# Performance work log

Hardware: AMD Instinct MI355X
Metric: run time of the kernel (lower is better)

The kernel has to match this reference:

```python
import jax, jax.numpy as jnp
import numpy as np

N = 200000      # nodes per graph
E = 6400000     # edges per graph
F_IN = 100      # node feature dim (GCNConv(100,16))
HID = 16
NC = 2
STRIDE = 20     # log_softmax(...)[::20]
M = N // STRIDE # rows fed to the MLP head


def _gcn(x, src, dst, W1, b1, W2, b2):
    """PyG-style GCNConv x2: add self loops, sym-normalize, linear -> aggregate -> bias."""
    n = x.shape[0]
    loops = jnp.arange(n)
    s = jnp.concatenate([src, loops])
    d = jnp.concatenate([dst, loops])
    deg = jax.ops.segment_sum(jnp.ones(s.shape[0], dtype=x.dtype), d, num_segments=n)
    dinv = jnp.where(deg > 0, jax.lax.rsqrt(deg), 0.0)
    norm = (dinv[s] * dinv[d])[:, None]  # [E+n, 1]
    h = x @ W1                                    # [n, 16]
    h = jax.ops.segment_sum(norm * h[s], d, num_segments=n) + b1
    h = jax.nn.relu(h)  # dropout is identity in eval mode
    h = h @ W2                                    # [n, 2]
    h = jax.ops.segment_sum(norm * h[s], d, num_segments=n) + b2
    return jax.nn.log_softmax(h, axis=1)[::STRIDE]  # [n/20, 2]


def setup_inputs() -> dict:
    key = jax.random.key(0)
    ks = jax.random.split(key, 24)
    inp = {
        'batch1_edge_index': jax.random.randint(ks[0], (2, E), 0, N),
        'batch1_x': jax.random.normal(ks[1], (N, F_IN), dtype=jnp.float32),
        'batch2_edge_index': jax.random.randint(ks[2], (2, E), 0, N),
        'batch2_x': jax.random.normal(ks[3], (N, F_IN), dtype=jnp.float32),
        'transE_input': jax.random.uniform(ks[4], (M,), dtype=jnp.float32),
        'ComplEx_input': jax.random.uniform(ks[5], (M,), dtype=jnp.float32),
        'path_input': jax.random.uniform(ks[6], (M,), dtype=jnp.float32),
        'edit_input': jax.random.uniform(ks[7], (M,), dtype=jnp.float32),
    }
    s = 0.1
    inp['gh_W1'] = jax.random.normal(ks[8], (F_IN, HID), dtype=jnp.float32) * s
    inp['gh_b1'] = jnp.zeros((HID,), dtype=jnp.float32)
    inp['gh_W2'] = jax.random.normal(ks[9], (HID, NC), dtype=jnp.float32) * s
    inp['gh_b2'] = jnp.zeros((NC,), dtype=jnp.float32)
    inp['gt_W1'] = jax.random.normal(ks[10], (F_IN, HID), dtype=jnp.float32) * s
    inp['gt_b1'] = jnp.zeros((HID,), dtype=jnp.float32)
    inp['gt_W2'] = jax.random.normal(ks[11], (HID, NC), dtype=jnp.float32) * s
    inp['gt_b2'] = jnp.zeros((NC,), dtype=jnp.float32)
    inp['m_W1'] = jax.random.normal(ks[12], (5, 80), dtype=jnp.float32) * s
    inp['m_b1'] = jnp.zeros((80,), dtype=jnp.float32)
    inp['m_W2'] = jax.random.normal(ks[13], (80, 10), dtype=jnp.float32) * s
    inp['m_b2'] = jnp.zeros((10,), dtype=jnp.float32)
    inp['m_W3'] = jax.random.normal(ks[14], (10, 1), dtype=jnp.float32) * s
    inp['m_b3'] = jnp.zeros((1,), dtype=jnp.float32)
    return inp


def reference(batch1_edge_index, batch1_x, batch2_edge_index, batch2_x,
              transE_input, ComplEx_input, path_input, edit_input,
              gh_W1, gh_b1, gh_W2, gh_b2,
              gt_W1, gt_b1, gt_W2, gt_b2,
              m_W1, m_b1, m_W2, m_b2, m_W3, m_b3):
    gcnh_out = _gcn(batch1_x, batch1_edge_index[0], batch1_edge_index[1],
                    gh_W1, gh_b1, gh_W2, gh_b2)
    # gcnt_out is computed in the original forward but never used in the output
    gcnt_out = _gcn(batch2_x, batch2_edge_index[0], batch2_edge_index[1],
                    gt_W1, gt_b1, gt_W2, gt_b2)
    BP_input = jnp.concatenate(
        [transE_input[:, None], ComplEx_input[:, None], path_input[:, None], gcnh_out], axis=1)  # [M, 5]
    # NOTE: original computes mean/std normalization then OVERWRITES it with
    # min_max_normalize(BP_input); we faithfully apply only global min-max.
    mn, mx = jnp.min(BP_input), jnp.max(BP_input)
    BP_norm = (BP_input - mn) / (mx - mn)
    h = jax.nn.relu(BP_norm @ m_W1 + m_b1)
    h = jax.nn.relu(h @ m_W2 + m_b2)
    out = jax.nn.sigmoid(h @ m_W3 + m_b3)  # [M, 1]
    return out
```

## Files before the change

kernel.cpp:

```cpp
#include <hip/hip_runtime.h>
#include <math.h>

#define NN 200000
#define NE 6400000
#define FIN 100
#define MR 10000
#define BSH 14
#define NBK 13
#define NSB 1563
#define EPB 4096
#define CAP1E 544768
#define SBB 133
#define CAP2E 4864
#define SCAP 360448
#define STCAP 5120

static __device__ __forceinline__ unsigned enc_f(float f){
  unsigned u = __float_as_uint(f);
  return (u & 0x80000000u) ? ~u : (u | 0x80000000u);
}
static __device__ __forceinline__ float dec_f(unsigned u){
  return (u & 0x80000000u) ? __uint_as_float(u ^ 0x80000000u) : __uint_as_float(~u);
}
static __device__ __forceinline__ unsigned short f2bf(float f){
  unsigned u = __float_as_uint(f);
  return (unsigned short)((u + 0x7fffu + ((u >> 16) & 1u)) >> 16);
}
static __device__ __forceinline__ float bf2f(unsigned short h){
  return __uint_as_float(((unsigned)h) << 16);
}

__global__ void k_init(int* bcur1, int* bcur2, float* gacc, unsigned* mm, unsigned* scnt){
  int i = blockIdx.x*blockDim.x + threadIdx.x;
  if(i < NBK) bcur1[i] = i*CAP1E;
  if(i < NSB) bcur2[i] = i*CAP2E;
  if(i < 2*MR) gacc[i] = 0.f;
  if(i == 0){ mm[0] = 0xFFFFFFFFu; mm[1] = 0u; scnt[0] = 0u; }
}

__global__ __launch_bounds__(256) void k_stageA(const int* __restrict__ src,
                                                const int* __restrict__ dst,
                                                int* __restrict__ bcur1,
                                                unsigned* __restrict__ bucket1){
  __shared__ unsigned stage[EPB];
  __shared__ unsigned char binOf[EPB];
  __shared__ int cnt[4][NBK];
  __shared__ int tot[NBK], bst[NBK], woff[4][NBK], gbase[NBK];
  int t = threadIdx.x;
  int w = t >> 6;
  int ebase = blockIdx.x*EPB;
  int nEdge = min(EPB, NE - ebase);
  if(t < 4*NBK) ((int*)cnt)[t] = 0;
  __syncthreads();
  unsigned pk[16]; int bb[16], rr[16];
  const int4* s4 = (const int4*)(src + ebase);
  const int4* d4 = (const int4*)(dst + ebase);
  #pragma unroll
  for(int j=0;j<4;j++){
    int q = t + j*256, eo = q*4;
    if(eo < nEdge){
      int4 s = s4[q]; int4 d = d4[q];
      int ds[4] = {d.x,d.y,d.z,d.w}, ss[4] = {s.x,s.y,s.z,s.w};
      #pragma unroll
      for(int k=0;k<4;k++){
        int b = ds[k]>>BSH;
        pk[j*4+k] = ((unsigned)(ds[k] & 16383) << 18) | (unsigned)ss[k];
        bb[j*4+k] = b;
        rr[j*4+k] = atomicAdd(&cnt[w][b], 1);
      }
    } else {
      rr[j*4+0]=rr[j*4+1]=rr[j*4+2]=rr[j*4+3] = -1;
    }
  }
  __syncthreads();
  if(t < NBK){
    int s = 0;
    #pragma unroll
    for(int wv=0; wv<4; wv++){ woff[wv][t] = s; s += cnt[wv][t]; }
    tot[t] = s;
  }
  __syncthreads();
  if(t == 0){
    int run = 0;
    #pragma unroll
    for(int b=0;b<NBK;b++){ bst[b] = run; run += tot[b]; }
  }
  __syncthreads();
  if(t < NBK && tot[t]) gbase[t] = atomicAdd(&bcur1[t], tot[t]);
  #pragma unroll
  for(int j=0;j<16;j++){
    if(rr[j] >= 0){
      int b = bb[j];
      int p = bst[b] + woff[w][b] + rr[j];
      stage[p] = pk[j]; binOf[p] = (unsigned char)b;
    }
  }
  __syncthreads();
  for(int k=t; k<nEdge; k+=256){
    int b = binOf[k];
    bucket1[gbase[b] + (k - bst[b])] = stage[k];
  }
}

__global__ __launch_bounds__(256) void k_stageB(const unsigned* __restrict__ bucket1,
                                                const int* __restrict__ bcur1,
                                                int* __restrict__ bcur2,
                                                unsigned* __restrict__ bucket2,
                                                unsigned* __restrict__ sed,
                                                unsigned* __restrict__ scnt){
  __shared__ unsigned stage[EPB];
  __shared__ unsigned char binOf[EPB];
  __shared__ int cnt[128], bst[128], gbase[128];
  __shared__ unsigned sbuf[384];
  __shared__ int slds, sgbase;
  int t = threadIdx.x;
  int b = blockIdx.x / SBB;
  int chunk = blockIdx.x % SBB;
  int cntb = bcur1[b] - b*CAP1E;
  int el = chunk*EPB;
  int nEdge = min(EPB, cntb - el);
  if(nEdge <= 0) return;
  if(t < 128) cnt[t] = 0;
  if(t == 0) slds = 0;
  __syncthreads();
  int t20 = (20 - (4*b) % 20) % 20;
  unsigned pk2[16]; int ln[16], rr[16];
  const uint4* e4 = (const uint4*)(bucket1 + (size_t)b*CAP1E + el);
  #pragma unroll
  for(int j=0;j<4;j++){
    int q = t + j*256, eo = q*4;
    uint4 e = make_uint4(0,0,0,0);
    if(eo < nEdge) e = e4[q];
    unsigned ev[4] = {e.x, e.y, e.z, e.w};
    #pragma unroll
    for(int k=0;k<4;k++){
      int idx = j*4+k;
      if(eo + k < nEdge){
        unsigned p = ev[k];
        unsigned dl14 = p >> 18;
        int bin = (int)(dl14 >> 7);
        pk2[idx] = ((dl14 & 127u) << 18) | (p & 0x3FFFFu);
        ln[idx] = bin;
        rr[idx] = atomicAdd(&cnt[bin], 1);
        if((int)(dl14 % 20u) == t20){
          int sp = atomicAdd(&slds, 1);
          if(sp < 384){
            unsigned sidx = (unsigned)((b*16384 + (int)dl14) / 20);
            sbuf[sp] = (sidx << 18) | (p & 0x3FFFFu);
          }
        }
      } else rr[idx] = -1;
    }
  }
  __syncthreads();
  if(t == 0){
    int run = 0;
    for(int i=0;i<128;i++){ bst[i] = run; run += cnt[i]; }
    if(slds > 384) slds = 384;
    sgbase = (slds > 0) ? (int)atomicAdd(scnt, (unsigned)slds) : 0;
  }
  __syncthreads();
  if(t < 128 && cnt[t]){
    int sbg = (b<<7) + t;
    gbase[t] = atomicAdd(&bcur2[sbg], cnt[t]);
  }
  #pragma unroll
  for(int j=0;j<16;j++){
    if(rr[j] >= 0){
      int p = bst[ln[j]] + rr[j];
      stage[p] = pk2[j]; binOf[p] = (unsigned char)ln[j];
    }
  }
  __syncthreads();
  for(int k=t; k<nEdge; k+=256){
    int bin = binOf[k];
    bucket2[gbase[bin] + (k - bst[bin])] = stage[k];
  }
  for(int k=t; k<slds; k+=256){
    int gp = sgbase + k;
    if(gp < SCAP) sed[gp] = sbuf[k];
  }
}

__global__ __launch_bounds__(256) void k_cnt(const unsigned* __restrict__ bucket2,
                                             const int* __restrict__ bcur2,
                                             float* __restrict__ dinv){
  __shared__ int c[128];
  int sb = blockIdx.x, t = threadIdx.x;
  if(t < 128) c[t] = 0;
  __syncthreads();
  int e0 = sb*CAP2E, e1 = bcur2[sb];
  for(int i=e0+t; i<e1; i+=256){
    unsigned pkv = bucket2[i];
    atomicAdd(&c[pkv>>18], 1);
  }
  __syncthreads();
  if(t < 128){
    int g = sb*128 + t;
    if(g < NN) dinv[g] = rsqrtf((float)(c[t] + 1));
  }
}

__global__ __launch_bounds__(256) void k_xw1(const float* __restrict__ x,
                                             const float* __restrict__ W1,
                                             const float* __restrict__ dinv,
                                             unsigned short* __restrict__ h1b){
  int row = blockIdx.x*256 + threadIdx.x;
  if(row >= NN) return;
  const float4* xr = (const float4*)(x + (size_t)row*FIN);
  float acc[16];
  #pragma unroll
  for(int c=0;c<16;c++) acc[c] = 0.f;
  #pragma unroll 5
  for(int kk=0;kk<25;kk++){
    float4 xv = xr[kk];
    const float* w = W1 + kk*4*16;
    #pragma unroll
    for(int c=0;c<16;c++){
      acc[c] += xv.x*w[c] + xv.y*w[16+c] + xv.z*w[32+c] + xv.w*w[48+c];
    }
  }
  float dv = dinv[row];
  unsigned p[8];
  #pragma unroll
  for(int c=0;c<8;c++){
    p[c] = (unsigned)f2bf(acc[2*c]*dv) | ((unsigned)f2bf(acc[2*c+1]*dv) << 16);
  }
  uint4* o = (uint4*)(h1b + (size_t)row*16);
  o[0] = make_uint4(p[0],p[1],p[2],p[3]);
  o[1] = make_uint4(p[4],p[5],p[6],p[7]);
}

__global__ __launch_bounds__(512) void k_aggfused(const unsigned* __restrict__ bucket2,
                                                  const int* __restrict__ bcur2,
                                                  const float* __restrict__ dinv,
                                                  const unsigned short* __restrict__ h1b,
                                                  const float* __restrict__ b1,
                                                  const float* __restrict__ W2,
                                                  float* __restrict__ h2s){
  __shared__ unsigned srt[STCAP];
  __shared__ int cnt[128], coff[129], cur[128];
  __shared__ int wsum0;
  int t = threadIdx.x, sb = blockIdx.x;
  int e0 = sb*CAP2E, e1 = bcur2[sb];
  int n  = e1 - e0;
  bool ok = (n <= STCAP);
  if(t < 128) cnt[t] = 0;
  __syncthreads();

  if(ok){
    unsigned er[10];
    #pragma unroll
    for(int k=0;k<10;k++){
      int i = e0 + t + k*512;
      if(i < e1){
        unsigned p = bucket2[i];
        er[k] = p;
        atomicAdd(&cnt[p>>18], 1);
      } else er[k] = 0xFFFFFFFFu;
    }
    __syncthreads();
    int v = (t<128) ? cnt[t] : 0;
    int s = v;
    #pragma unroll
    for(int o=1;o<64;o<<=1){
      int u = __shfl_up(s, o, 64);
      if((t&63) >= o) s += u;
    }
    if(t == 63) wsum0 = s;
    __syncthreads();
    if(t < 128){
      int ex = s - v + ((t>=64) ? wsum0 : 0);
      coff[t] = ex; cur[t] = ex;
    }
    if(t == 0) coff[128] = n;
    __syncthreads();
    #pragma unroll
    for(int k=0;k<10;k++){
      if(er[k] != 0xFFFFFFFFu){
        int p = atomicAdd(&cur[er[k]>>18], 1);
        srt[p] = er[k] & 0x3FFFFu;
      }
    }
    __syncthreads();
    int grp = t>>3, f2 = t&7;
    const unsigned* h1u = (const unsigned*)h1b;
    for(int nd=grp; nd<128; nd+=64){
      int g = sb*128 + nd;
      if(g >= NN) continue;
      int s0 = coff[nd], s1 = coff[nd+1];
      unsigned su = h1u[(size_t)g*8 + f2];
      float acc0 = bf2f((unsigned short)su);
      float acc1 = bf2f((unsigned short)(su>>16));
      int j = s0;
      for(; j+4 <= s1; j+=4){
        unsigned a0=srt[j], a1=srt[j+1], a2=srt[j+2], a3=srt[j+3];
        unsigned u0 = h1u[a0*8+f2], u1 = h1u[a1*8+f2];
        unsigned u2 = h1u[a2*8+f2], u3 = h1u[a3*8+f2];
        acc0 += (bf2f((unsigned short)u0) + bf2f((unsigned short)u1))
              + (bf2f((unsigned short)u2) + bf2f((unsigned short)u3));
        acc1 += (bf2f((unsigned short)(u0>>16)) + bf2f((unsigned short)(u1>>16)))
              + (bf2f((unsigned short)(u2>>16)) + bf2f((unsigned short)(u3>>16)));
      }
      for(; j<s1; j++){
        unsigned u = h1u[srt[j]*8+f2];
        acc0 += bf2f((unsigned short)u);
        acc1 += bf2f((unsigned short)(u>>16));
      }
      float dvd = dinv[g];
      float r0 = fmaxf(dvd*acc0 + b1[2*f2],   0.f);
      float r1 = fmaxf(dvd*acc1 + b1[2*f2+1], 0.f);
      float p0 = r0*W2[(2*f2)*2+0] + r1*W2[(2*f2+1)*2+0];
      float p1 = r0*W2[(2*f2)*2+1] + r1*W2[(2*f2+1)*2+1];
      #pragma unroll
      for(int o=4;o>0;o>>=1){
        p0 += __shfl_xor(p0, o, 8);
        p1 += __shfl_xor(p1, o, 8);
      }
      if(f2 == 0){
        h2s[g*2+0] = dvd * p0;
        h2s[g*2+1] = dvd * p1;
      }
    }
  } else {
    float* accf = (float*)srt;
    for(int i=t; i<2048; i+=512) accf[i] = 0.f;
    __syncthreads();
    int grp = t>>4, f = t&15;
    for(int i=e0+grp; i<e1; i+=32){
      unsigned pkv = bucket2[i];
      atomicAdd(&accf[(pkv>>18)*16 + f], bf2f(h1b[(size_t)(pkv & 0x3FFFFu)*16 + f]));
    }
    __syncthreads();
    for(int nd=grp; nd<128; nd+=32){
      int g = sb*128 + nd;
      if(g >= NN) continue;
      float dvd = dinv[g];
      float acc = accf[nd*16 + f] + bf2f(h1b[(size_t)g*16 + f]);
      float r = fmaxf(dvd*acc + b1[f], 0.f);
      float p0 = r * W2[f*2+0];
      float p1 = r * W2[f*2+1];
      #pragma unroll
      for(int o=8;o>0;o>>=1){
        p0 += __shfl_xor(p0, o, 16);
        p1 += __shfl_xor(p1, o, 16);
      }
      if(f == 0){
        h2s[g*2+0] = dvd * p0;
        h2s[g*2+1] = dvd * p1;
      }
    }
  }
}

__global__ __launch_bounds__(256) void k_agg2s(const unsigned* __restrict__ sed,
                                               const unsigned* __restrict__ scnt,
                                               const float* __restrict__ h2s,
                                               float* __restrict__ gacc){
  int total = (int)scnt[0];
  if(total > SCAP) total = SCAP;
  const float2* h2v = (const float2*)h2s;
  for(int i = blockIdx.x*256 + threadIdx.x; i < total; i += gridDim.x*256){
    unsigned p = sed[i];
    int idx = (int)(p >> 18);
    int srcn = (int)(p & 0x3FFFFu);
    float2 v = h2v[srcn];
    atomicAdd(&gacc[idx*2+0], v.x);
    atomicAdd(&gacc[idx*2+1], v.y);
  }
}

__global__ __launch_bounds__(256) void k_post(const float* __restrict__ gacc,
                                              const float* __restrict__ h2s,
                                              const float* __restrict__ dinv,
                                              const float* __restrict__ b2,
                                              const float* __restrict__ t1,
                                              const float* __restrict__ t2,
                                              const float* __restrict__ t3,
                                              float* __restrict__ gout,
                                              unsigned* __restrict__ mm){
  int i = blockIdx.x*256 + threadIdx.x;
  float lo = 3.4e38f, hi = -3.4e38f;
  if(i < MR){
    int g = i*20;
    float dvd = dinv[g];
    float o0 = dvd*(gacc[i*2+0] + h2s[g*2+0]) + b2[0];
    float o1 = dvd*(gacc[i*2+1] + h2s[g*2+1]) + b2[1];
    float m = fmaxf(o0, o1);
    float lse = m + logf(expf(o0-m) + expf(o1-m));
    float g0 = o0 - lse, g1 = o1 - lse;
    gout[i*2+0] = g0; gout[i*2+1] = g1;
    float a = t1[i], bb = t2[i], c = t3[i];
    lo = fminf(fminf(a,bb), fminf(c, fminf(g0,g1)));
    hi = fmaxf(fmaxf(a,bb), fmaxf(c, fmaxf(g0,g1)));
  }
  #pragma unroll
  for(int o=32;o>0;o>>=1){
    lo = fminf(lo, __shfl_xor(lo, o, 64));
    hi = fmaxf(hi, __shfl_xor(hi, o, 64));
  }
  __shared__ float slo[4], shi[4];
  int w = threadIdx.x >> 6, l = threadIdx.x & 63;
  if(l == 0){ slo[w] = lo; shi[w] = hi; }
  __syncthreads();
  if(threadIdx.x == 0){
    for(int j=1;j<4;j++){ lo = fminf(lo, slo[j]); hi = fmaxf(hi, shi[j]); }
    atomicMin(&mm[0], enc_f(lo));
    atomicMax(&mm[1], enc_f(hi));
  }
}

__global__ __launch_bounds__(256) void k_mlp(const float* __restrict__ t1, const float* __restrict__ t2,
                                             const float* __restrict__ t3, const float* __restrict__ g,
                                             const unsigned* __restrict__ mm,
                                             const float* __restrict__ W1, const float* __restrict__ b1,
                                             const float* __restrict__ W2, const float* __restrict__ b2,
                                             const float* __restrict__ W3, const float* __restrict__ b3,
                                             float* __restrict__ out){
  int i = blockIdx.x*256 + threadIdx.x;
  if(i >= MR) return;
  float mn = dec_f(mm[0]), mx = dec_f(mm[1]);
  float sc = 1.f/(mx - mn);
  float in[5];
  in[0] = (t1[i]   - mn)*sc;
  in[1] = (t2[i]   - mn)*sc;
  in[2] = (t3[i]   - mn)*sc;
  in[3] = (g[2*i]  - mn)*sc;
  in[4] = (g[2*i+1]- mn)*sc;
  float a[80];
  #pragma unroll
  for(int j=0;j<80;j++){
    float s = b1[j];
    #pragma unroll
    for(int k=0;k<5;k++) s += in[k]*W1[k*80+j];
    a[j] = fmaxf(s, 0.f);
  }
  float h[10];
  #pragma unroll
  for(int j=0;j<10;j++){
    float s = b2[j];
    #pragma unroll
    for(int k=0;k<80;k++) s += a[k]*W2[k*10+j];
    h[j] = fmaxf(s, 0.f);
  }
  float o = b3[0];
  #pragma unroll
  for(int k=0;k<10;k++) o += h[k]*W3[k];
  out[i] = 1.f/(1.f + expf(-o));
}

extern "C" void kernel_launch(void* const* d_in, const int* in_sizes, int n_in,
                              void* d_out, int out_size, void* d_ws, size_t ws_size,
                              hipStream_t stream) {
  (void)in_sizes; (void)n_in; (void)out_size; (void)ws_size;
  const int*   eidx    = (const int*)  d_in[0];
  const int*   src     = eidx;
  const int*   dst     = eidx + NE;
  const float* x       = (const float*)d_in[1];
  const float* transE  = (const float*)d_in[4];
  const float* ComplEx = (const float*)d_in[5];
  const float* path    = (const float*)d_in[6];
  const float* ghW1    = (const float*)d_in[8];
  const float* ghb1    = (const float*)d_in[9];
  const float* ghW2    = (const float*)d_in[10];
  const float* ghb2    = (const float*)d_in[11];
  const float* mW1     = (const float*)d_in[16];
  const float* mb1     = (const float*)d_in[17];
  const float* mW2     = (const float*)d_in[18];
  const float* mb2     = (const float*)d_in[19];
  const float* mW3     = (const float*)d_in[20];
  const float* mb3     = (const float*)d_in[21];
  float* out = (float*)d_out;

  char* w = (char*)d_ws;
  size_t off = 0;
  auto alloc = [&](size_t bytes)->void*{
    void* p = w + off;
    off += (bytes + 255) & ~(size_t)255;
    return p;
  };
  unsigned* bucket1 = (unsigned*)alloc((size_t)NBK*CAP1E*4);
  unsigned* bucket2 = (unsigned*)alloc((size_t)NSB*CAP2E*4);
  float*    dinv    = (float*)   alloc((size_t)NN*4);
  unsigned short* h1b = (unsigned short*)alloc((size_t)NN*16*2);
  float*    h2s     = (float*)   alloc((size_t)NN*2*4);
  float*    gacc    = (float*)   alloc((size_t)MR*2*4);
  float*    gout    = (float*)   alloc((size_t)MR*2*4);
  unsigned* sed     = (unsigned*)alloc((size_t)SCAP*4);
  int*      bcur1   = (int*)     alloc(64*4);
  int*      bcur2   = (int*)     alloc((size_t)(NSB+1)*4);
  unsigned* mm      = (unsigned*)alloc(256);
  unsigned* scnt    = (unsigned*)alloc(256);

  const int SA_BLOCKS = (NE + EPB - 1)/EPB;
  const int SB_BLOCKS = NBK*SBB;

  k_init    <<<(2*MR+255)/256, 256, 0, stream>>>(bcur1, bcur2, gacc, mm, scnt);
  k_stageA  <<<SA_BLOCKS, 256, 0, stream>>>(src, dst, bcur1, bucket1);
  k_stageB  <<<SB_BLOCKS, 256, 0, stream>>>(bucket1, bcur1, bcur2, bucket2, sed, scnt);
  k_cnt     <<<NSB, 256, 0, stream>>>(bucket2, bcur2, dinv);
  k_xw1     <<<(NN+255)/256, 256, 0, stream>>>(x, ghW1, dinv, h1b);
  k_aggfused<<<NSB, 512, 0, stream>>>(bucket2, bcur2, dinv, h1b, ghb1, ghW2, h2s);
  k_agg2s   <<<512, 256, 0, stream>>>(sed, scnt, h2s, gacc);
  k_post    <<<(MR+255)/256, 256, 0, stream>>>(gacc, h2s, dinv, ghb2,
                                               transE, ComplEx, path, gout, mm);
  k_mlp     <<<(MR+255)/256, 256, 0, stream>>>(transE, ComplEx, path, gout, mm,
                                               mW1, mb1, mW2, mb2, mW3, mb3, out);
}
```

Baseline: 445.6 us.

## Split bf16 node features into two 8-feature planes and gather them in two passes

The h1 feature table is stored as two separate planes of 8 bf16 features each (16 bytes per node per plane) instead of one interleaved 32-byte row. The fused aggregation gathers each plane in its own pass, with 4 lanes per node and an 8-way unrolled loop, so each pass touches a smaller working set that fits in cache better. k_xw1 now assigns 4 lanes per row, splitting the K dimension and combining partial sums with shuffles, which improves coalescing of x reads. The cost is a second gather pass over the edge list and an extra block barrier.

```diff
diff --git a/kernel.cpp b/kernel.cpp
--- a/kernel.cpp
+++ b/kernel.cpp
@@ -29,6 +29,8 @@
 static __device__ __forceinline__ float bf2f(unsigned short h){
   return __uint_as_float(((unsigned)h) << 16);
 }
+static __device__ __forceinline__ float bflo(unsigned u){ return bf2f((unsigned short)u); }
+static __device__ __forceinline__ float bfhi(unsigned u){ return bf2f((unsigned short)(u>>16)); }
 
 __global__ void k_init(int* bcur1, int* bcur2, float* gacc, unsigned* mm, unsigned* scnt){
   int i = blockIdx.x*blockDim.x + threadIdx.x;
@@ -205,30 +207,33 @@
                                              const float* __restrict__ W1,
                                              const float* __restrict__ dinv,
                                              unsigned short* __restrict__ h1b){
-  int row = blockIdx.x*256 + threadIdx.x;
+  int t = threadIdx.x;
+  int l = t & 3;
+  int row = blockIdx.x*64 + (t>>2);
   if(row >= NN) return;
   const float4* xr = (const float4*)(x + (size_t)row*FIN);
   float acc[16];
   #pragma unroll
   for(int c=0;c<16;c++) acc[c] = 0.f;
-  #pragma unroll 5
-  for(int kk=0;kk<25;kk++){
+  for(int kk=l; kk<25; kk+=4){
     float4 xv = xr[kk];
-    const float* w = W1 + kk*4*16;
+    const float* w = W1 + kk*64;
     #pragma unroll
     for(int c=0;c<16;c++){
       acc[c] += xv.x*w[c] + xv.y*w[16+c] + xv.z*w[32+c] + xv.w*w[48+c];
     }
   }
+  #pragma unroll
+  for(int o=2;o>0;o>>=1){
+    #pragma unroll
+    for(int c=0;c<16;c++) acc[c] += __shfl_xor(acc[c], o, 4);
+  }
   float dv = dinv[row];
-  unsigned p[8];
-  #pragma unroll
-  for(int c=0;c<8;c++){
-    p[c] = (unsigned)f2bf(acc[2*c]*dv) | ((unsigned)f2bf(acc[2*c+1]*dv) << 16);
-  }
-  uint4* o = (uint4*)(h1b + (size_t)row*16);
-  o[0] = make_uint4(p[0],p[1],p[2],p[3]);
-  o[1] = make_uint4(p[4],p[5],p[6],p[7]);
+  unsigned p0 = (unsigned)f2bf(acc[4*l]*dv)   | ((unsigned)f2bf(acc[4*l+1]*dv) << 16);
+  unsigned p1 = (unsigned)f2bf(acc[4*l+2]*dv) | ((unsigned)f2bf(acc[4*l+3]*dv) << 16);
+  unsigned* plane = (unsigned*)h1b + (size_t)(l>>1)*NN*4;
+  uint2* o2 = (uint2*)(plane + (size_t)row*4 + (l&1)*2);
+  *o2 = make_uint2(p0, p1);
 }
 
 __global__ __launch_bounds__(512) void k_aggfused(const unsigned* __restrict__ bucket2,
@@ -283,41 +288,81 @@
       }
     }
     __syncthreads();
-    int grp = t>>3, f2 = t&7;
-    const unsigned* h1u = (const unsigned*)h1b;
-    for(int nd=grp; nd<128; nd+=64){
-      int g = sb*128 + nd;
-      if(g >= NN) continue;
-      int s0 = coff[nd], s1 = coff[nd+1];
-      unsigned su = h1u[(size_t)g*8 + f2];
-      float acc0 = bf2f((unsigned short)su);
-      float acc1 = bf2f((unsigned short)(su>>16));
+
+    int grp = t>>2, f = t&3;
+    int g = sb*128 + grp;
+    bool live = (g < NN);
+    int s0 = 0, s1 = 0;
+    if(live){ s0 = coff[grp]; s1 = coff[grp+1]; }
+    float a00=0.f, a01=0.f, a10=0.f, a11=0.f;
+    const unsigned* h1u0 = (const unsigned*)h1b;
+    const unsigned* h1u1 = h1u0 + (size_t)NN*4;
+
+    if(live){
+      unsigned su = h1u0[(size_t)g*4 + f];
+      a00 = bflo(su); a01 = bfhi(su);
       int j = s0;
+      for(; j+8 <= s1; j+=8){
+        unsigned b0=srt[j],b1_=srt[j+1],b2=srt[j+2],b3=srt[j+3];
+        unsigned b4=srt[j+4],b5=srt[j+5],b6=srt[j+6],b7=srt[j+7];
+        unsigned u0=h1u0[b0*4+f], u1=h1u0[b1_*4+f], u2=h1u0[b2*4+f], u3=h1u0[b3*4+f];
+        unsigned u4=h1u0[b4*4+f], u5=h1u0[b5*4+f], u6=h1u0[b6*4+f], u7=h1u0[b7*4+f];
+        a00 += ((bflo(u0)+bflo(u1)) + (bflo(u2)+bflo(u3)))
+             + ((bflo(u4)+bflo(u5)) + (bflo(u6)+bflo(u7)));
+        a01 += ((bfhi(u0)+bfhi(u1)) + (bfhi(u2)+bfhi(u3)))
+             + ((bfhi(u4)+bfhi(u5)) + (bfhi(u6)+bfhi(u7)));
+      }
       for(; j+4 <= s1; j+=4){
-        unsigned a0=srt[j], a1=srt[j+1], a2=srt[j+2], a3=srt[j+3];
-        unsigned u0 = h1u[a0*8+f2], u1 = h1u[a1*8+f2];
-        unsigned u2 = h1u[a2*8+f2], u3 = h1u[a3*8+f2];
-        acc0 += (bf2f((unsigned short)u0) + bf2f((unsigned short)u1))
-              + (bf2f((unsigned short)u2) + bf2f((unsigned short)u3));
-        acc1 += (bf2f((unsigned short)(u0>>16)) + bf2f((unsigned short)(u1>>16)))
-              + (bf2f((unsigned short)(u2>>16)) + bf2f((unsigned short)(u3>>16)));
+        unsigned b0=srt[j],b1_=srt[j+1],b2=srt[j+2],b3=srt[j+3];
+        unsigned u0=h1u0[b0*4+f], u1=h1u0[b1_*4+f], u2=h1u0[b2*4+f], u3=h1u0[b3*4+f];
+        a00 += (bflo(u0)+bflo(u1)) + (bflo(u2)+bflo(u3));
+        a01 += (bfhi(u0)+bfhi(u1)) + (bfhi(u2)+bfhi(u3));
       }
       for(; j<s1; j++){
-        unsigned u = h1u[srt[j]*8+f2];
-        acc0 += bf2f((unsigned short)u);
-        acc1 += bf2f((unsigned short)(u>>16));
+        unsigned u = h1u0[srt[j]*4+f];
+        a00 += bflo(u); a01 += bfhi(u);
+      }
+    }
+    __syncthreads();
+    if(live){
+      unsigned su = h1u1[(size_t)g*4 + f];
+      a10 = bflo(su); a11 = bfhi(su);
+      int j = s0;
+      for(; j+8 <= s1; j+=8){
+        unsigned b0=srt[j],b1_=srt[j+1],b2=srt[j+2],b3=srt[j+3];
+        unsigned b4=srt[j+4],b5=srt[j+5],b6=srt[j+6],b7=srt[j+7];
+        unsigned u0=h1u1[b0*4+f], u1=h1u1[b1_*4+f], u2=h1u1[b2*4+f], u3=h1u1[b3*4+f];
+        unsigned u4=h1u1[b4*4+f], u5=h1u1[b5*4+f], u6=h1u1[b6*4+f], u7=h1u1[b7*4+f];
+        a10 += ((bflo(u0)+bflo(u1)) + (bflo(u2)+bflo(u3)))
+             + ((bflo(u4)+bflo(u5)) + (bflo(u6)+bflo(u7)));
+        a11 += ((bfhi(u0)+bfhi(u1)) + (bfhi(u2)+bfhi(u3)))
+             + ((bfhi(u4)+bfhi(u5)) + (bfhi(u6)+bfhi(u7)));
+      }
+      for(; j+4 <= s1; j+=4){
+        unsigned b0=srt[j],b1_=srt[j+1],b2=srt[j+2],b3=srt[j+3];
+        unsigned u0=h1u1[b0*4+f], u1=h1u1[b1_*4+f], u2=h1u1[b2*4+f], u3=h1u1[b3*4+f];
+        a10 += (bflo(u0)+bflo(u1)) + (bflo(u2)+bflo(u3));
+        a11 += (bfhi(u0)+bfhi(u1)) + (bfhi(u2)+bfhi(u3));
+      }
+      for(; j<s1; j++){
+        unsigned u = h1u1[srt[j]*4+f];
+        a10 += bflo(u); a11 += bfhi(u);
       }
       float dvd = dinv[g];
-      float r0 = fmaxf(dvd*acc0 + b1[2*f2],   0.f);
-      float r1 = fmaxf(dvd*acc1 + b1[2*f2+1], 0.f);
-      float p0 = r0*W2[(2*f2)*2+0] + r1*W2[(2*f2+1)*2+0];
-      float p1 = r0*W2[(2*f2)*2+1] + r1*W2[(2*f2+1)*2+1];
+      float r00 = fmaxf(dvd*a00 + b1[2*f],   0.f);
+      float r01 = fmaxf(dvd*a01 + b1[2*f+1], 0.f);
+      float r10 = fmaxf(dvd*a10 + b1[8+2*f], 0.f);
+      float r11 = fmaxf(dvd*a11 + b1[9+2*f], 0.f);
+      float p0 = r00*W2[(2*f)*2+0] + r01*W2[(2*f+1)*2+0]
+               + r10*W2[(8+2*f)*2+0] + r11*W2[(9+2*f)*2+0];
+      float p1 = r00*W2[(2*f)*2+1] + r01*W2[(2*f+1)*2+1]
+               + r10*W2[(8+2*f)*2+1] + r11*W2[(9+2*f)*2+1];
       #pragma unroll
-      for(int o=4;o>0;o>>=1){
-        p0 += __shfl_xor(p0, o, 8);
-        p1 += __shfl_xor(p1, o, 8);
-      }
-      if(f2 == 0){
+      for(int o=2;o>0;o>>=1){
+        p0 += __shfl_xor(p0, o, 4);
+        p1 += __shfl_xor(p1, o, 4);
+      }
+      if(f == 0){
         h2s[g*2+0] = dvd * p0;
         h2s[g*2+1] = dvd * p1;
       }
@@ -327,16 +372,22 @@
     for(int i=t; i<2048; i+=512) accf[i] = 0.f;
     __syncthreads();
     int grp = t>>4, f = t&15;
+    int pl = f>>3, fi = f&7;
+    const unsigned* h1u = (const unsigned*)h1b + (size_t)pl*NN*4;
     for(int i=e0+grp; i<e1; i+=32){
       unsigned pkv = bucket2[i];
-      atomicAdd(&accf[(pkv>>18)*16 + f], bf2f(h1b[(size_t)(pkv & 0x3FFFFu)*16 + f]));
+      unsigned u = h1u[(size_t)(pkv & 0x3FFFFu)*4 + (fi>>1)];
+      float v = (fi&1) ? bfhi(u) : bflo(u);
+      atomicAdd(&accf[(pkv>>18)*16 + f], v);
     }
     __syncthreads();
     for(int nd=grp; nd<128; nd+=32){
       int g = sb*128 + nd;
       if(g >= NN) continue;
+      unsigned su = h1u[(size_t)g*4 + (fi>>1)];
+      float sv = (fi&1) ? bfhi(su) : bflo(su);
       float dvd = dinv[g];
-      float acc = accf[nd*16 + f] + bf2f(h1b[(size_t)g*16 + f]);
+      float acc = accf[nd*16 + f] + sv;
       float r = fmaxf(dvd*acc + b1[f], 0.f);
       float p0 = r * W2[f*2+0];
       float p1 = r * W2[f*2+1];
@@ -499,7 +550,7 @@
   k_stageA  <<<SA_BLOCKS, 256, 0, stream>>>(src, dst, bcur1, bucket1);
   k_stageB  <<<SB_BLOCKS, 256, 0, stream>>>(bucket1, bcur1, bcur2, bucket2, sed, scnt);
   k_cnt     <<<NSB, 256, 0, stream>>>(bucket2, bcur2, dinv);
-  k_xw1     <<<(NN+255)/256, 256, 0, stream>>>(x, ghW1, dinv, h1b);
+  k_xw1     <<<(NN+63)/64, 256, 0, stream>>>(x, ghW1, dinv, h1b);
   k_aggfused<<<NSB, 512, 0, stream>>>(bucket2, bcur2, dinv, h1b, ghb1, ghW2, h2s);
   k_agg2s   <<<512, 256, 0, stream>>>(sed, scnt, h2s, gacc);
   k_post    <<<(MR+255)/256, 256, 0, stream>>>(gacc, h2s, dinv, ghb2,
```

After: 571.5 us. 28.3% more time.
